# Kernel tuning notes

Measured on AMD Instinct MI355X. Metric: run time of the kernel, lower is better.

Reference implementation:

```python
import jax, jax.numpy as jnp
import numpy as np

N = 100000
E = 1000000
H = 128
DF = 64
TOTAL_GENES = 20000
NUM_PERTS = 5000


def setup_inputs() -> dict:
    key = jax.random.key(0)
    ks = jax.random.split(key, 32)
    d_in1 = DF + H  # all_feat=True: concat raw feats with gene embedding

    def g(k, shape, scale=0.05):
        return jax.random.normal(k, shape, dtype=jnp.float32) * scale

    inp = {
        'x': jax.random.normal(ks[0], (N, DF), dtype=jnp.float32),
        'edge_index': jax.random.randint(ks[1], (2, E), 0, N),
        'edge_attr': jax.random.normal(ks[2], (E, 1), dtype=jnp.float32),
        'pert': jax.random.randint(ks[3], (N,), 0, NUM_PERTS),
        'ctrl': jax.random.normal(ks[4], (N, 1), dtype=jnp.float32),
        'pos': jax.random.randint(ks[5], (N,), 0, TOTAL_GENES),
        # learned parameters
        'gene_table': g(ks[6], (TOTAL_GENES, H), 1.0),
        'pert_table': g(ks[7], (NUM_PERTS, H), 1.0),
        'W1': g(ks[8], (d_in1, H)), 'a_src1': g(ks[9], (H,)), 'a_dst1': g(ks[10], (H,)), 'b1': g(ks[11], (H,)),
        'Wl1': g(ks[12], (d_in1, H)), 'bl1': g(ks[13], (H,)),
        'W2': g(ks[14], (H, H)), 'a_src2': g(ks[15], (H,)), 'a_dst2': g(ks[16], (H,)), 'b2': g(ks[17], (H,)),
        'Wl2': g(ks[18], (H, H)), 'bl2': g(ks[19], (H,)),
        'Wm1': g(ks[20], (2 * H + 1, H // 2)), 'bm1': g(ks[21], (H // 2,)),
        'Wm2': g(ks[22], (H // 2, 1)), 'bm2': g(ks[23], (1,)),
    }
    return inp


def gat_conv(x, src, dst, W, a_src, a_dst, b, n_nodes):
    # PyG GATConv, heads=1, concat=False, negative_slope=0.2, add_self_loops
    h = x @ W                         # [N, H]
    asrc = h @ a_src                  # [N]
    adst = h @ a_dst                  # [N]
    loop = jnp.arange(n_nodes)
    s = jnp.concatenate([src, loop])  # [E+N]
    d = jnp.concatenate([dst, loop])
    e = jax.nn.leaky_relu(asrc[s] + adst[d], negative_slope=0.2)
    m = jax.ops.segment_max(e, d, num_segments=n_nodes)
    ex = jnp.exp(e - m[d])
    denom = jax.ops.segment_sum(ex, d, num_segments=n_nodes)
    alpha = ex / (denom[d] + 1e-16)
    out = jax.ops.segment_sum(h[s] * alpha[:, None], d, num_segments=n_nodes)
    return out + b


def _forward(x, edge_attr, ctrl, gene_table, pert_table,
             W1, a_src1, a_dst1, b1, Wl1, bl1,
             W2, a_src2, a_dst2, b2, Wl2, bl2,
             Wm1, bm1, Wm2, bm2,
             edge_index, pert, pos):
    src, dst = edge_index[0], edge_index[1]
    # gene embedding with max_norm=True (rows renormed to norm <= 1.0)
    pe = gene_table[pos]
    nrm = jnp.linalg.norm(pe, axis=-1, keepdims=True)
    pe = jnp.where(nrm > 1.0, pe / (nrm + 1e-7), pe)
    h = jnp.concatenate([x, pe], axis=1)            # [N, DF+H]
    h = gat_conv(h, src, dst, W1, a_src1, a_dst1, b1, x.shape[0]) + h @ Wl1 + bl1
    h = jax.nn.relu(h)
    h = gat_conv(h, src, dst, W2, a_src2, a_dst2, b2, x.shape[0]) + h @ Wl2 + bl2
    z = jnp.concatenate([h, ctrl, pert_table[pert]], axis=1)  # [N, 2H+1]
    z = jax.nn.relu(z @ Wm1 + bm1)
    z = jax.nn.relu(z @ Wm2 + bm2)
    return z.squeeze(1)


def reference(x, edge_index, edge_attr, pert, ctrl, pos,
              gene_table, pert_table,
              W1, a_src1, a_dst1, b1, Wl1, bl1,
              W2, a_src2, a_dst2, b2, Wl2, bl2,
              Wm1, bm1, Wm2, bm2):
    return _forward(x, edge_attr, ctrl, gene_table, pert_table,
                    W1, a_src1, a_dst1, b1, Wl1, bl1,
                    W2, a_src2, a_dst2, b2, Wl2, bl2,
                    Wm1, bm1, Wm2, bm2,
                    edge_index, pert, pos)
```

## Files before the change

kernel.cpp:

```cpp
#include <hip/hip_runtime.h>
#include <hip/hip_bf16.h>

typedef __bf16 bf16;
typedef __bf16 bf16x8 __attribute__((ext_vector_type(8)));
typedef __bf16 bf16x4 __attribute__((ext_vector_type(4)));
typedef __bf16 bf16x2 __attribute__((ext_vector_type(2)));
typedef float f32x4 __attribute__((ext_vector_type(4)));

#define CAP 48

__device__ __forceinline__ float b2f(bf16 v) { return (float)v; }
__device__ __forceinline__ bf16 f2b(float v) { return (bf16)v; }

__device__ __forceinline__ float leaky(float x) { return fmaxf(x, 0.2f * x); }

__device__ __forceinline__ bf16x8 zero8() {
    bf16x8 v;
    #pragma unroll
    for (int j = 0; j < 8; ++j) v[j] = (bf16)0.0f;
    return v;
}

__device__ __forceinline__ void swizzle_one(const float* __restrict__ W, bf16* __restrict__ dst,
                                            int f, int NT, int Kreal, int C) {
    int kb = f / (NT * 64);
    int rem = f % (NT * 64);
    int nt = rem / 64;
    int ln = rem % 64;
    int q = ln >> 4, m = ln & 15;
    int c = nt * 16 + m;
    bf16x8 v;
    #pragma unroll
    for (int j = 0; j < 8; ++j) {
        int k = kb * 32 + q * 8 + j;
        v[j] = (k < Kreal) ? f2b(W[k * C + c]) : (bf16)0.0f;
    }
    *reinterpret_cast<bf16x8*>(dst + f * 8) = v;
}

__global__ void h0_prep_kernel(const float* __restrict__ x,
                               const float* __restrict__ gene_table,
                               const int* __restrict__ pos,
                               bf16* __restrict__ h0, int n,
                               const float* __restrict__ W1, const float* __restrict__ Wl1,
                               const float* __restrict__ W2, const float* __restrict__ Wl2,
                               const float* __restrict__ Wm1,
                               bf16* __restrict__ w1s, bf16* __restrict__ wl1s,
                               bf16* __restrict__ w2s, bf16* __restrict__ wl2s,
                               bf16* __restrict__ wm1s,
                               const int* __restrict__ e_src, const int* __restrict__ e_dst,
                               int* __restrict__ cnt, int* __restrict__ colidx,
                               int e, int nbsc, int nboth) {
    int g5 = blockIdx.x / 5, r5 = blockIdx.x % 5;
    if (r5 == 0) {
        if (g5 >= nbsc) return;
        int i = g5 * blockDim.x + threadIdx.x;
        if (i < e) {
            int d = __builtin_nontemporal_load(e_dst + i);
            int s = __builtin_nontemporal_load(e_src + i);
            int k = atomicAdd(&cnt[d], 1);
            if (k < CAP) __builtin_nontemporal_store(s, colidx + d * CAP + k);
        }
        return;
    }
    int ob = g5 * 4 + (r5 - 1);
    if (ob >= nboth) return;
    if (ob < 49) {
        int g = ob * blockDim.x + threadIdx.x;
        if (g < 3072)        swizzle_one(W1,  w1s,  g,          8, 192, 128);
        else if (g < 6144)   swizzle_one(Wl1, wl1s, g - 3072,   8, 192, 128);
        else if (g < 8192)   swizzle_one(W2,  w2s,  g - 6144,   8, 128, 128);
        else if (g < 10240)  swizzle_one(Wl2, wl2s, g - 8192,   8, 128, 128);
        else if (g < 12544)  swizzle_one(Wm1, wm1s, g - 10240,  4, 257,  64);
        return;
    }
    int wid = (ob - 49) * 8 + (threadIdx.x >> 5);
    int l = threadIdx.x & 31;
    if (wid >= n) return;
    const float* g = gene_table + (long long)pos[wid] * 128;
    float4 p = reinterpret_cast<const float4*>(g)[l];
    float ss = p.x * p.x + p.y * p.y + p.z * p.z + p.w * p.w;
    #pragma unroll
    for (int o = 16; o; o >>= 1) ss += __shfl_xor(ss, o);
    float nrm = sqrtf(ss);
    float sc = nrm > 1.0f ? 1.0f / (nrm + 1e-7f) : 1.0f;
    bf16* orow = h0 + (long long)wid * 192;
    float2 xv = reinterpret_cast<const float2*>(x + (long long)wid * 64)[l];
    bf16x2 xb; xb[0] = f2b(xv.x); xb[1] = f2b(xv.y);
    *reinterpret_cast<bf16x2*>(orow + 2 * l) = xb;
    bf16x4 gb;
    gb[0] = f2b(p.x * sc); gb[1] = f2b(p.y * sc);
    gb[2] = f2b(p.z * sc); gb[3] = f2b(p.w * sc);
    *reinterpret_cast<bf16x4*>(orow + 64 + 4 * l) = gb;
}

template <int KB>
__global__ __launch_bounds__(256) void gemm_dual_kernel(
    const bf16* __restrict__ A, int lda,
    const bf16* __restrict__ Wg, const bf16* __restrict__ Wl,
    const float* __restrict__ bias_l,
    bf16* __restrict__ outg, bf16* __restrict__ outl, int ldo, int nrows,
    const float* __restrict__ attn_s, const float* __restrict__ attn_d,
    float* __restrict__ asrc, float* __restrict__ adst) {
    const int NTT = 8;
    __shared__ float sA[64][2];
    int tid = threadIdx.x;
    int wave = tid >> 6, lane = tid & 63;
    int q = lane >> 4, m = lane & 15;
    int nt0 = (wave & 1) * 4;
    long long row_base = (long long)blockIdx.x * 64 + (wave >> 1) * 32;
    long long r0 = row_base + m;
    long long r1 = row_base + 16 + m;
    bool v0 = r0 < nrows, v1 = r1 < nrows;

    f32x4 accg[2][4], accl[2][4];
    #pragma unroll
    for (int t = 0; t < 2; ++t)
        #pragma unroll
        for (int nt = 0; nt < 4; ++nt) {
            f32x4 z = {0.f, 0.f, 0.f, 0.f};
            accg[t][nt] = z; accl[t][nt] = z;
        }

    bf16x8 b0 = v0 ? *reinterpret_cast<const bf16x8*>(A + r0 * lda + q * 8) : zero8();
    bf16x8 b1 = v1 ? *reinterpret_cast<const bf16x8*>(A + r1 * lda + q * 8) : zero8();
    #pragma unroll
    for (int kb = 0; kb < KB; ++kb) {
        bf16x8 nb0, nb1;
        if (kb + 1 < KB) {
            nb0 = v0 ? *reinterpret_cast<const bf16x8*>(A + r0 * lda + (kb + 1) * 32 + q * 8) : zero8();
            nb1 = v1 ? *reinterpret_cast<const bf16x8*>(A + r1 * lda + (kb + 1) * 32 + q * 8) : zero8();
        }
        #pragma unroll
        for (int nt = 0; nt < 4; ++nt) {
            bf16x8 wg = *reinterpret_cast<const bf16x8*>(Wg + ((kb * NTT + nt0 + nt) * 64 + lane) * 8);
            bf16x8 wl = *reinterpret_cast<const bf16x8*>(Wl + ((kb * NTT + nt0 + nt) * 64 + lane) * 8);
            accg[0][nt] = __builtin_amdgcn_mfma_f32_16x16x32_bf16(wg, b0, accg[0][nt], 0, 0, 0);
            accg[1][nt] = __builtin_amdgcn_mfma_f32_16x16x32_bf16(wg, b1, accg[1][nt], 0, 0, 0);
            accl[0][nt] = __builtin_amdgcn_mfma_f32_16x16x32_bf16(wl, b0, accl[0][nt], 0, 0, 0);
            accl[1][nt] = __builtin_amdgcn_mfma_f32_16x16x32_bf16(wl, b1, accl[1][nt], 0, 0, 0);
        }
        b0 = nb0; b1 = nb1;
    }
    #pragma unroll
    for (int t = 0; t < 2; ++t) {
        long long row = t ? r1 : r0;
        if (row < nrows) {
            #pragma unroll
            for (int nt = 0; nt < 4; ++nt) {
                int c0 = (nt0 + nt) * 16 + q * 4;
                bf16x4 og, ol;
                #pragma unroll
                for (int r = 0; r < 4; ++r) {
                    og[r] = f2b(accg[t][nt][r]);
                    ol[r] = f2b(accl[t][nt][r] + bias_l[c0 + r]);
                }
                *reinterpret_cast<bf16x4*>(outg + row * ldo + c0) = og;
                *reinterpret_cast<bf16x4*>(outl + row * ldo + c0) = ol;
            }
        }
    }
    float svt[2], dvt[2];
    #pragma unroll
    for (int t = 0; t < 2; ++t) {
        float sv = 0.f, dv = 0.f;
        #pragma unroll
        for (int nt = 0; nt < 4; ++nt) {
            int c0 = (nt0 + nt) * 16 + q * 4;
            #pragma unroll
            for (int r = 0; r < 4; ++r) {
                float v = accg[t][nt][r];
                sv = fmaf(v, attn_s[c0 + r], sv);
                dv = fmaf(v, attn_d[c0 + r], dv);
            }
        }
        sv += __shfl_xor(sv, 16); sv += __shfl_xor(sv, 32);
        dv += __shfl_xor(dv, 16); dv += __shfl_xor(dv, 32);
        svt[t] = sv; dvt[t] = dv;
        if ((wave & 1) == 0 && q == 0) {
            int rloc = (wave >> 1) * 32 + t * 16 + m;
            sA[rloc][0] = sv; sA[rloc][1] = dv;
        }
    }
    __syncthreads();
    #pragma unroll
    for (int t = 0; t < 2; ++t) {
        long long row = t ? r1 : r0;
        if ((wave & 1) == 1 && q == 0 && row < nrows) {
            int rloc = (wave >> 1) * 32 + t * 16 + m;
            asrc[row] = svt[t] + sA[rloc][0];
            adst[row] = dvt[t] + sA[rloc][1];
        }
    }
}

template <int KB, int NT>
__global__ __launch_bounds__(256) void gemm_mlp_kernel(
    const bf16* __restrict__ A, int lda,
    const bf16* __restrict__ Wsw,
    const float* __restrict__ bias, int nrows,
    const float* __restrict__ Wm2, const float* __restrict__ bm2,
    float* __restrict__ out_final) {
    int tid = threadIdx.x;
    int wave = tid >> 6, lane = tid & 63;
    int q = lane >> 4, m = lane & 15;
    long long row_base = (long long)blockIdx.x * 128 + wave * 32;
    long long r0 = row_base + m;
    long long r1 = row_base + 16 + m;
    bool v0 = r0 < nrows, v1 = r1 < nrows;

    f32x4 acc[2][NT];
    #pragma unroll
    for (int t = 0; t < 2; ++t)
        #pragma unroll
        for (int nt = 0; nt < NT; ++nt) {
            f32x4 z = {0.f, 0.f, 0.f, 0.f};
            acc[t][nt] = z;
        }

    bf16x8 b0 = v0 ? *reinterpret_cast<const bf16x8*>(A + r0 * lda + q * 8) : zero8();
    bf16x8 b1 = v1 ? *reinterpret_cast<const bf16x8*>(A + r1 * lda + q * 8) : zero8();
    #pragma unroll
    for (int kb = 0; kb < KB; ++kb) {
        bf16x8 nb0, nb1;
        if (kb + 1 < KB) {
            nb0 = v0 ? *reinterpret_cast<const bf16x8*>(A + r0 * lda + (kb + 1) * 32 + q * 8) : zero8();
            nb1 = v1 ? *reinterpret_cast<const bf16x8*>(A + r1 * lda + (kb + 1) * 32 + q * 8) : zero8();
        }
        #pragma unroll
        for (int nt = 0; nt < NT; ++nt) {
            bf16x8 w = *reinterpret_cast<const bf16x8*>(Wsw + ((kb * NT + nt) * 64 + lane) * 8);
            acc[0][nt] = __builtin_amdgcn_mfma_f32_16x16x32_bf16(w, b0, acc[0][nt], 0, 0, 0);
            acc[1][nt] = __builtin_amdgcn_mfma_f32_16x16x32_bf16(w, b1, acc[1][nt], 0, 0, 0);
        }
        b0 = nb0; b1 = nb1;
    }
    #pragma unroll
    for (int t = 0; t < 2; ++t) {
        float sv = 0.f;
        #pragma unroll
        for (int nt = 0; nt < NT; ++nt) {
            int c0 = nt * 16 + q * 4;
            #pragma unroll
            for (int r = 0; r < 4; ++r) {
                float v = fmaxf(acc[t][nt][r] + bias[c0 + r], 0.0f);
                sv = fmaf(v, Wm2[c0 + r], sv);
            }
        }
        sv += __shfl_xor(sv, 16); sv += __shfl_xor(sv, 32);
        long long row = t ? r1 : r0;
        if (q == 0 && row < nrows) out_final[row] = fmaxf(sv + bm2[0], 0.0f);
    }
}

__global__ __launch_bounds__(256, 2) void gat_edge_kernel(
                                const int* __restrict__ cnt, const int* __restrict__ colidx,
                                const float* __restrict__ asrc, const float* __restrict__ adst,
                                const bf16* __restrict__ hgat, const bf16* __restrict__ hlin,
                                const float* __restrict__ b_gat, int relu,
                                bf16* __restrict__ out, int ldo, int n,
                                const float* __restrict__ ctrl,
                                const float* __restrict__ pert_table,
                                const int* __restrict__ pert) {
    int d = blockIdx.x * 8 + (threadIdx.x >> 5);
    int lane = threadIdx.x & 31;
    if (d >= n) return;
    float ad = adst[d];
    float e_self = leaky(asrc[d] + ad);
    int cn = cnt[d]; if (cn > CAP) cn = CAP;
    bool val0 = lane < cn;
    bool val1 = lane + 32 < cn;
    int sj0 = val0 ? __builtin_nontemporal_load(colidx + d * CAP + lane) : d;
    int sj1 = val1 ? __builtin_nontemporal_load(colidx + d * CAP + 32 + lane) : d;
    float ej0 = val0 ? leaky(asrc[sj0] + ad) : -1e30f;
    float ej1 = val1 ? leaky(asrc[sj1] + ad) : -1e30f;
    float mx = fmaxf(ej0, ej1);
    #pragma unroll
    for (int o = 16; o; o >>= 1) mx = fmaxf(mx, __shfl_xor(mx, o, 32));
    mx = fmaxf(mx, e_self);
    float wj0 = val0 ? __expf(ej0 - mx) : 0.0f;
    float wj1 = val1 ? __expf(ej1 - mx) : 0.0f;
    float ws = __expf(e_self - mx);
    float sm = wj0 + wj1;
    #pragma unroll
    for (int o = 16; o; o >>= 1) sm += __shfl_xor(sm, o, 32);
    float den = sm + ws;
    bf16x4 hl = *reinterpret_cast<const bf16x4*>(hlin + (long long)d * 128 + 4 * lane);
    float4 bg = *reinterpret_cast<const float4*>(b_gat + 4 * lane);
    bf16x4 hd = *reinterpret_cast<const bf16x4*>(hgat + (long long)d * 128 + 4 * lane);
    float acc0 = ws * b2f(hd[0]), acc1 = ws * b2f(hd[1]);
    float acc2 = ws * b2f(hd[2]), acc3 = ws * b2f(hd[3]);
    int c1 = cn < 32 ? cn : 32;
    for (int j = 0; j < c1; j += 4) {
        int s0 = __shfl(sj0, j, 32), s1 = __shfl(sj0, j + 1, 32);
        int s2 = __shfl(sj0, j + 2, 32), s3 = __shfl(sj0, j + 3, 32);
        float w0 = __shfl(wj0, j, 32), w1 = __shfl(wj0, j + 1, 32);
        float w2 = __shfl(wj0, j + 2, 32), w3 = __shfl(wj0, j + 3, 32);
        bf16x4 h0v = *reinterpret_cast<const bf16x4*>(hgat + (long long)s0 * 128 + 4 * lane);
        bf16x4 h1v = *reinterpret_cast<const bf16x4*>(hgat + (long long)s1 * 128 + 4 * lane);
        bf16x4 h2v = *reinterpret_cast<const bf16x4*>(hgat + (long long)s2 * 128 + 4 * lane);
        bf16x4 h3v = *reinterpret_cast<const bf16x4*>(hgat + (long long)s3 * 128 + 4 * lane);
        acc0 = fmaf(w0, b2f(h0v[0]), acc0); acc1 = fmaf(w0, b2f(h0v[1]), acc1);
        acc2 = fmaf(w0, b2f(h0v[2]), acc2); acc3 = fmaf(w0, b2f(h0v[3]), acc3);
        acc0 = fmaf(w1, b2f(h1v[0]), acc0); acc1 = fmaf(w1, b2f(h1v[1]), acc1);
        acc2 = fmaf(w1, b2f(h1v[2]), acc2); acc3 = fmaf(w1, b2f(h1v[3]), acc3);
        acc0 = fmaf(w2, b2f(h2v[0]), acc0); acc1 = fmaf(w2, b2f(h2v[1]), acc1);
        acc2 = fmaf(w2, b2f(h2v[2]), acc2); acc3 = fmaf(w2, b2f(h2v[3]), acc3);
        acc0 = fmaf(w3, b2f(h3v[0]), acc0); acc1 = fmaf(w3, b2f(h3v[1]), acc1);
        acc2 = fmaf(w3, b2f(h3v[2]), acc2); acc3 = fmaf(w3, b2f(h3v[3]), acc3);
    }
    for (int j = 32; j < cn; j += 4) {
        int s0 = __shfl(sj1, j - 32, 32), s1 = __shfl(sj1, j - 31, 32);
        int s2 = __shfl(sj1, j - 30, 32), s3 = __shfl(sj1, j - 29, 32);
        float w0 = __shfl(wj1, j - 32, 32), w1 = __shfl(wj1, j - 31, 32);
        float w2 = __shfl(wj1, j - 30, 32), w3 = __shfl(wj1, j - 29, 32);
        bf16x4 h0v = *reinterpret_cast<const bf16x4*>(hgat + (long long)s0 * 128 + 4 * lane);
        bf16x4 h1v = *reinterpret_cast<const bf16x4*>(hgat + (long long)s1 * 128 + 4 * lane);
        bf16x4 h2v = *reinterpret_cast<const bf16x4*>(hgat + (long long)s2 * 128 + 4 * lane);
        bf16x4 h3v = *reinterpret_cast<const bf16x4*>(hgat + (long long)s3 * 128 + 4 * lane);
        acc0 = fmaf(w0, b2f(h0v[0]), acc0); acc1 = fmaf(w0, b2f(h0v[1]), acc1);
        acc2 = fmaf(w0, b2f(h0v[2]), acc2); acc3 = fmaf(w0, b2f(h0v[3]), acc3);
        acc0 = fmaf(w1, b2f(h1v[0]), acc0); acc1 = fmaf(w1, b2f(h1v[1]), acc1);
        acc2 = fmaf(w1, b2f(h1v[2]), acc2); acc3 = fmaf(w1, b2f(h1v[3]), acc3);
        acc0 = fmaf(w2, b2f(h2v[0]), acc0); acc1 = fmaf(w2, b2f(h2v[1]), acc1);
        acc2 = fmaf(w2, b2f(h2v[2]), acc2); acc3 = fmaf(w2, b2f(h2v[3]), acc3);
        acc0 = fmaf(w3, b2f(h3v[0]), acc0); acc1 = fmaf(w3, b2f(h3v[1]), acc1);
        acc2 = fmaf(w3, b2f(h3v[2]), acc2); acc3 = fmaf(w3, b2f(h3v[3]), acc3);
    }
    float inv = 1.0f / den;
    float o0 = acc0 * inv + bg.x + b2f(hl[0]);
    float o1 = acc1 * inv + bg.y + b2f(hl[1]);
    float o2 = acc2 * inv + bg.z + b2f(hl[2]);
    float o3 = acc3 * inv + bg.w + b2f(hl[3]);
    if (relu) {
        o0 = fmaxf(o0, 0.0f); o1 = fmaxf(o1, 0.0f);
        o2 = fmaxf(o2, 0.0f); o3 = fmaxf(o3, 0.0f);
    }
    bf16* orow = out + (long long)d * ldo;
    bf16x4 ov; ov[0] = f2b(o0); ov[1] = f2b(o1); ov[2] = f2b(o2); ov[3] = f2b(o3);
    *reinterpret_cast<bf16x4*>(orow + 4 * lane) = ov;
    if (pert) {
        const float* p = pert_table + (long long)pert[d] * 128;
        if (lane == 0) orow[128] = f2b(ctrl[d]);
        orow[129 + lane] = f2b(p[lane]);
        orow[161 + lane] = f2b(p[32 + lane]);
        orow[193 + lane] = f2b(p[64 + lane]);
        orow[225 + lane] = f2b(p[96 + lane]);
        if (lane < 31) orow[257 + lane] = (bf16)0.0f;
    }
}

extern "C" void kernel_launch(void* const* d_in, const int* in_sizes, int n_in,
                              void* d_out, int out_size, void* d_ws, size_t ws_size,
                              hipStream_t stream) {
    const int N = in_sizes[0] / 64;
    const int E = in_sizes[1] / 2;

    const float* x          = (const float*)d_in[0];
    const int*   ei         = (const int*)d_in[1];
    const int*   e_src      = ei;
    const int*   e_dst      = ei + E;
    const int*   pert       = (const int*)d_in[3];
    const float* ctrl       = (const float*)d_in[4];
    const int*   pos        = (const int*)d_in[5];
    const float* gene_table = (const float*)d_in[6];
    const float* pert_table = (const float*)d_in[7];
    const float* W1   = (const float*)d_in[8];
    const float* a_s1 = (const float*)d_in[9];
    const float* a_d1 = (const float*)d_in[10];
    const float* b1   = (const float*)d_in[11];
    const float* Wl1  = (const float*)d_in[12];
    const float* bl1  = (const float*)d_in[13];
    const float* W2   = (const float*)d_in[14];
    const float* a_s2 = (const float*)d_in[15];
    const float* a_d2 = (const float*)d_in[16];
    const float* b2   = (const float*)d_in[17];
    const float* Wl2  = (const float*)d_in[18];
    const float* bl2  = (const float*)d_in[19];
    const float* Wm1  = (const float*)d_in[20];
    const float* bm1  = (const float*)d_in[21];
    const float* Wm2  = (const float*)d_in[22];
    const float* bm2  = (const float*)d_in[23];

    char* ws = (char*)d_ws;
    size_t off = 0;
    auto alloc = [&](size_t bytes) {
        char* p = ws + off;
        off = (off + bytes + 255) & ~(size_t)255;
        return p;
    };
    bf16* hgat   = (bf16*)alloc((size_t)N * 128 * 2);
    bf16* hlin   = (bf16*)alloc((size_t)N * 128 * 2);
    bf16* h0     = (bf16*)alloc((size_t)N * 192 * 2);
    bf16* h1     = (bf16*)alloc((size_t)N * 128 * 2);
    bf16* zbuf   = h0;
    float* asrc  = (float*)alloc((size_t)N * 4);
    float* adst  = (float*)alloc((size_t)N * 4);
    int* cnt     = (int*)alloc((size_t)N * 4);
    int* colidx  = (int*)alloc((size_t)N * CAP * 4);
    bf16* w1s    = (bf16*)alloc((size_t)3072 * 8 * 2);
    bf16* wl1s   = (bf16*)alloc((size_t)3072 * 8 * 2);
    bf16* w2s    = (bf16*)alloc((size_t)2048 * 8 * 2);
    bf16* wl2s   = (bf16*)alloc((size_t)2048 * 8 * 2);
    bf16* wm1s   = (bf16*)alloc((size_t)2304 * 8 * 2);
    (void)ws_size; (void)n_in; (void)out_size;

    float* out = (float*)d_out;

    const int NBH8 = (N + 7) / 8;
    const int NBOTH = 49 + NBH8;
    const int NBSC = (E + 255) / 256;
    const int NG5 = (NBSC > (NBOTH + 3) / 4) ? NBSC : (NBOTH + 3) / 4;
    const int NBFUSED = NG5 * 5;
    const int NBG64 = (N + 63) / 64;
    const int NBG128 = (N + 127) / 128;
    dim3 blk(256);
    dim3 gridWave((N + 7) / 8);

    hipMemsetAsync(cnt, 0, (size_t)N * 4, stream);
    hipLaunchKernelGGL(h0_prep_kernel, dim3(NBFUSED), blk, 0, stream,
                       x, gene_table, pos, h0, N,
                       W1, Wl1, W2, Wl2, Wm1, w1s, wl1s, w2s, wl2s, wm1s,
                       e_src, e_dst, cnt, colidx, E, NBSC, NBOTH);
    hipLaunchKernelGGL((gemm_dual_kernel<6>), dim3(NBG64), blk, 0, stream,
                       h0, 192, w1s, wl1s, bl1, hgat, hlin, 128, N,
                       a_s1, a_d1, asrc, adst);
    hipLaunchKernelGGL(gat_edge_kernel, gridWave, blk, 0, stream,
                       cnt, colidx, asrc, adst, hgat, hlin, b1, 1, h1, 128, N,
                       (const float*)nullptr, (const float*)nullptr, (const int*)nullptr);
    hipLaunchKernelGGL((gemm_dual_kernel<4>), dim3(NBG64), blk, 0, stream,
                       h1, 128, w2s, wl2s, bl2, hgat, hlin, 128, N,
                       a_s2, a_d2, asrc, adst);
    hipLaunchKernelGGL(gat_edge_kernel, gridWave, blk, 0, stream,
                       cnt, colidx, asrc, adst, hgat, hlin, b2, 0, zbuf, 288, N,
                       ctrl, pert_table, pert);
    hipLaunchKernelGGL((gemm_mlp_kernel<9, 4>), dim3(NBG128), blk, 0, stream,
                       zbuf, 288, wm1s, bm1, N, Wm2, bm2, out);
}
```

Before: 377.6 us.

## Fuse final MLP head into second GAT edge aggregation kernel

The second GAT edge kernel now stages each block's 8 output rows plus ctrl and perturbation embeddings in shared memory. It then runs the Wm1 MFMA GEMM and the Wm2 reduction in place, writing the final output directly. This removes the N×288 bf16 z buffer round-trip through global memory and one kernel launch. In exchange, half of each 16-row MFMA tile is wasted because a block covers only 8 nodes, and the kernel takes extra shared memory and two block barriers, which may lower occupancy.

Result: no change. 370.5 us (-1.9%).

```diff
diff --git a/kernel.cpp b/kernel.cpp
--- a/kernel.cpp
+++ b/kernel.cpp
@@ -194,65 +194,7 @@
     }
 }
 
-template <int KB, int NT>
-__global__ __launch_bounds__(256) void gemm_mlp_kernel(
-    const bf16* __restrict__ A, int lda,
-    const bf16* __restrict__ Wsw,
-    const float* __restrict__ bias, int nrows,
-    const float* __restrict__ Wm2, const float* __restrict__ bm2,
-    float* __restrict__ out_final) {
-    int tid = threadIdx.x;
-    int wave = tid >> 6, lane = tid & 63;
-    int q = lane >> 4, m = lane & 15;
-    long long row_base = (long long)blockIdx.x * 128 + wave * 32;
-    long long r0 = row_base + m;
-    long long r1 = row_base + 16 + m;
-    bool v0 = r0 < nrows, v1 = r1 < nrows;
-
-    f32x4 acc[2][NT];
-    #pragma unroll
-    for (int t = 0; t < 2; ++t)
-        #pragma unroll
-        for (int nt = 0; nt < NT; ++nt) {
-            f32x4 z = {0.f, 0.f, 0.f, 0.f};
-            acc[t][nt] = z;
-        }
-
-    bf16x8 b0 = v0 ? *reinterpret_cast<const bf16x8*>(A + r0 * lda + q * 8) : zero8();
-    bf16x8 b1 = v1 ? *reinterpret_cast<const bf16x8*>(A + r1 * lda + q * 8) : zero8();
-    #pragma unroll
-    for (int kb = 0; kb < KB; ++kb) {
-        bf16x8 nb0, nb1;
-        if (kb + 1 < KB) {
-            nb0 = v0 ? *reinterpret_cast<const bf16x8*>(A + r0 * lda + (kb + 1) * 32 + q * 8) : zero8();
-            nb1 = v1 ? *reinterpret_cast<const bf16x8*>(A + r1 * lda + (kb + 1) * 32 + q * 8) : zero8();
-        }
-        #pragma unroll
-        for (int nt = 0; nt < NT; ++nt) {
-            bf16x8 w = *reinterpret_cast<const bf16x8*>(Wsw + ((kb * NT + nt) * 64 + lane) * 8);
-            acc[0][nt] = __builtin_amdgcn_mfma_f32_16x16x32_bf16(w, b0, acc[0][nt], 0, 0, 0);
-            acc[1][nt] = __builtin_amdgcn_mfma_f32_16x16x32_bf16(w, b1, acc[1][nt], 0, 0, 0);
-        }
-        b0 = nb0; b1 = nb1;
-    }
-    #pragma unroll
-    for (int t = 0; t < 2; ++t) {
-        float sv = 0.f;
-        #pragma unroll
-        for (int nt = 0; nt < NT; ++nt) {
-            int c0 = nt * 16 + q * 4;
-            #pragma unroll
-            for (int r = 0; r < 4; ++r) {
-                float v = fmaxf(acc[t][nt][r] + bias[c0 + r], 0.0f);
-                sv = fmaf(v, Wm2[c0 + r], sv);
-            }
-        }
-        sv += __shfl_xor(sv, 16); sv += __shfl_xor(sv, 32);
-        long long row = t ? r1 : r0;
-        if (q == 0 && row < nrows) out_final[row] = fmaxf(sv + bm2[0], 0.0f);
-    }
-}
-
+template <int FUSED>
 __global__ __launch_bounds__(256, 2) void gat_edge_kernel(
                                 const int* __restrict__ cnt, const int* __restrict__ colidx,
                                 const float* __restrict__ asrc, const float* __restrict__ adst,
@@ -261,17 +203,26 @@
                                 bf16* __restrict__ out, int ldo, int n,
                                 const float* __restrict__ ctrl,
                                 const float* __restrict__ pert_table,
-                                const int* __restrict__ pert) {
+                                const int* __restrict__ pert,
+                                const bf16* __restrict__ wm1s,
+                                const float* __restrict__ bm1,
+                                const float* __restrict__ wm2,
+                                const float* __restrict__ bm2,
+                                float* __restrict__ out_final) {
+    __shared__ bf16 zs[16][296];
+    __shared__ float spart[8][4];
     int d = blockIdx.x * 8 + (threadIdx.x >> 5);
     int lane = threadIdx.x & 31;
-    if (d >= n) return;
-    float ad = adst[d];
-    float e_self = leaky(asrc[d] + ad);
-    int cn = cnt[d]; if (cn > CAP) cn = CAP;
+    bool act = d < n;
+    if (!FUSED && !act) return;
+    int da = act ? d : 0;
+    float ad = adst[da];
+    float e_self = leaky(asrc[da] + ad);
+    int cn = act ? cnt[da] : 0; if (cn > CAP) cn = CAP;
     bool val0 = lane < cn;
     bool val1 = lane + 32 < cn;
-    int sj0 = val0 ? __builtin_nontemporal_load(colidx + d * CAP + lane) : d;
-    int sj1 = val1 ? __builtin_nontemporal_load(colidx + d * CAP + 32 + lane) : d;
+    int sj0 = val0 ? __builtin_nontemporal_load(colidx + da * CAP + lane) : da;
+    int sj1 = val1 ? __builtin_nontemporal_load(colidx + da * CAP + 32 + lane) : da;
     float ej0 = val0 ? leaky(asrc[sj0] + ad) : -1e30f;
     float ej1 = val1 ? leaky(asrc[sj1] + ad) : -1e30f;
     float mx = fmaxf(ej0, ej1);
@@ -285,9 +236,9 @@
     #pragma unroll
     for (int o = 16; o; o >>= 1) sm += __shfl_xor(sm, o, 32);
     float den = sm + ws;
-    bf16x4 hl = *reinterpret_cast<const bf16x4*>(hlin + (long long)d * 128 + 4 * lane);
+    bf16x4 hl = *reinterpret_cast<const bf16x4*>(hlin + (long long)da * 128 + 4 * lane);
     float4 bg = *reinterpret_cast<const float4*>(b_gat + 4 * lane);
-    bf16x4 hd = *reinterpret_cast<const bf16x4*>(hgat + (long long)d * 128 + 4 * lane);
+    bf16x4 hd = *reinterpret_cast<const bf16x4*>(hgat + (long long)da * 128 + 4 * lane);
     float acc0 = ws * b2f(hd[0]), acc1 = ws * b2f(hd[1]);
     float acc2 = ws * b2f(hd[2]), acc3 = ws * b2f(hd[3]);
     int c1 = cn < 32 ? cn : 32;
@@ -336,17 +287,62 @@
         o0 = fmaxf(o0, 0.0f); o1 = fmaxf(o1, 0.0f);
         o2 = fmaxf(o2, 0.0f); o3 = fmaxf(o3, 0.0f);
     }
-    bf16* orow = out + (long long)d * ldo;
-    bf16x4 ov; ov[0] = f2b(o0); ov[1] = f2b(o1); ov[2] = f2b(o2); ov[3] = f2b(o3);
-    *reinterpret_cast<bf16x4*>(orow + 4 * lane) = ov;
-    if (pert) {
-        const float* p = pert_table + (long long)pert[d] * 128;
-        if (lane == 0) orow[128] = f2b(ctrl[d]);
-        orow[129 + lane] = f2b(p[lane]);
-        orow[161 + lane] = f2b(p[32 + lane]);
-        orow[193 + lane] = f2b(p[64 + lane]);
-        orow[225 + lane] = f2b(p[96 + lane]);
-        if (lane < 31) orow[257 + lane] = (bf16)0.0f;
+    if (!FUSED) {
+        bf16* orow = out + (long long)da * ldo;
+        bf16x4 ov; ov[0] = f2b(o0); ov[1] = f2b(o1); ov[2] = f2b(o2); ov[3] = f2b(o3);
+        *reinterpret_cast<bf16x4*>(orow + 4 * lane) = ov;
+        if (pert) {
+            const float* p = pert_table + (long long)pert[da] * 128;
+            if (lane == 0) orow[128] = f2b(ctrl[da]);
+            orow[129 + lane] = f2b(p[lane]);
+            orow[161 + lane] = f2b(p[32 + lane]);
+            orow[193 + lane] = f2b(p[64 + lane]);
+            orow[225 + lane] = f2b(p[96 + lane]);
+            if (lane < 31) orow[257 + lane] = (bf16)0.0f;
+        }
+        return;
+    }
+    int dl = threadIdx.x >> 5;
+    if (act) {
+        bf16x4 ov; ov[0] = f2b(o0); ov[1] = f2b(o1); ov[2] = f2b(o2); ov[3] = f2b(o3);
+        *reinterpret_cast<bf16x4*>(&zs[dl][4 * lane]) = ov;
+        const float* p = pert_table + (long long)pert[da] * 128;
+        if (lane == 0) zs[dl][128] = f2b(ctrl[da]);
+        zs[dl][129 + lane] = f2b(p[lane]);
+        zs[dl][161 + lane] = f2b(p[32 + lane]);
+        zs[dl][193 + lane] = f2b(p[64 + lane]);
+        zs[dl][225 + lane] = f2b(p[96 + lane]);
+        if (lane < 31) zs[dl][257 + lane] = (bf16)0.0f;
+    }
+    __syncthreads();
+    {
+        int tid = threadIdx.x;
+        int w = tid >> 6;
+        int lane64 = tid & 63;
+        int qq = lane64 >> 4, mm = lane64 & 15;
+        f32x4 macc = {0.f, 0.f, 0.f, 0.f};
+        #pragma unroll
+        for (int kb = 0; kb < 9; ++kb) {
+            bf16x8 zf = *reinterpret_cast<const bf16x8*>(&zs[mm][kb * 32 + qq * 8]);
+            bf16x8 wf = *reinterpret_cast<const bf16x8*>(wm1s + ((kb * 4 + w) * 64 + lane64) * 8);
+            macc = __builtin_amdgcn_mfma_f32_16x16x32_bf16(wf, zf, macc, 0, 0, 0);
+        }
+        float sv = 0.f;
+        int c0 = w * 16 + qq * 4;
+        #pragma unroll
+        for (int r = 0; r < 4; ++r) {
+            float v = fmaxf(macc[r] + bm1[c0 + r], 0.0f);
+            sv = fmaf(v, wm2[c0 + r], sv);
+        }
+        sv += __shfl_xor(sv, 16); sv += __shfl_xor(sv, 32);
+        if (qq == 0 && mm < 8) spart[mm][w] = sv;
+    }
+    __syncthreads();
+    if (threadIdx.x < 8) {
+        long long dd = (long long)blockIdx.x * 8 + threadIdx.x;
+        if (dd < n)
+            out_final[dd] = fmaxf(spart[threadIdx.x][0] + spart[threadIdx.x][1] +
+                                  spart[threadIdx.x][2] + spart[threadIdx.x][3] + bm2[0], 0.0f);
     }
 }
 
@@ -393,7 +389,6 @@
     bf16* hlin   = (bf16*)alloc((size_t)N * 128 * 2);
     bf16* h0     = (bf16*)alloc((size_t)N * 192 * 2);
     bf16* h1     = (bf16*)alloc((size_t)N * 128 * 2);
-    bf16* zbuf   = h0;
     float* asrc  = (float*)alloc((size_t)N * 4);
     float* adst  = (float*)alloc((size_t)N * 4);
     int* cnt     = (int*)alloc((size_t)N * 4);
@@ -413,7 +408,6 @@
     const int NG5 = (NBSC > (NBOTH + 3) / 4) ? NBSC : (NBOTH + 3) / 4;
     const int NBFUSED = NG5 * 5;
     const int NBG64 = (N + 63) / 64;
-    const int NBG128 = (N + 127) / 128;
     dim3 blk(256);
     dim3 gridWave((N + 7) / 8);
 
@@ -425,15 +419,16 @@
     hipLaunchKernelGGL((gemm_dual_kernel<6>), dim3(NBG64), blk, 0, stream,
                        h0, 192, w1s, wl1s, bl1, hgat, hlin, 128, N,
                        a_s1, a_d1, asrc, adst);
-    hipLaunchKernelGGL(gat_edge_kernel, gridWave, blk, 0, stream,
+    hipLaunchKernelGGL((gat_edge_kernel<0>), gridWave, blk, 0, stream,
                        cnt, colidx, asrc, adst, hgat, hlin, b1, 1, h1, 128, N,
-                       (const float*)nullptr, (const float*)nullptr, (const int*)nullptr);
+                       (const float*)nullptr, (const float*)nullptr, (const int*)nullptr,
+                       (const bf16*)nullptr, (const float*)nullptr,
+                       (const float*)nullptr, (const float*)nullptr, (float*)nullptr);
     hipLaunchKernelGGL((gemm_dual_kernel<4>), dim3(NBG64), blk, 0, stream,
                        h1, 128, w2s, wl2s, bl2, hgat, hlin, 128, N,
                        a_s2, a_d2, asrc, adst);
-    hipLaunchKernelGGL(gat_edge_kernel, gridWave, blk, 0, stream,
-                       cnt, colidx, asrc, adst, hgat, hlin, b2, 0, zbuf, 288, N,
-                       ctrl, pert_table, pert);
-    hipLaunchKernelGGL((gemm_mlp_kernel<9, 4>), dim3(NBG128), blk, 0, stream,
-                       zbuf, 288, wm1s, bm1, N, Wm2, bm2, out);
-}
+    hipLaunchKernelGGL((gat_edge_kernel<1>), gridWave, blk, 0, stream,
+                       cnt, colidx, asrc, adst, hgat, hlin, b2, 0, h1, 128, N,
+                       ctrl, pert_table, pert,
+                       (const bf16*)wm1s, bm1, Wm2, bm2, out);
+}
```
